# Kernel optimization log

Measured on AMD Instinct MI355X. Metric: run time of the kernel, lower is better.

The kernel has to match this reference:

```python
import jax, jax.numpy as jnp
import numpy as np

SIGMA = 1.0          # influence distance of kernel points
KERNEL_RADIUS = 1.0  # radius within which kernel points live


def setup_inputs() -> dict:
    key = jax.random.key(0)
    k0, k1, k2, k3, k4 = jax.random.split(key, 5)
    B, M, K_NB, D_IN, D_OUT, K_PTS = 4, 16384, 32, 64, 64, 15
    X = jax.random.normal(k0, (B, M, 3), dtype=jnp.float32)          # point coords
    F = jax.random.normal(k1, (B, M, D_IN), dtype=jnp.float32)        # point features
    N = jax.random.randint(k2, (B, M, K_NB), 0, M)                    # neighbor indices
    Q = jax.random.uniform(k3, (K_PTS, 3), minval=-KERNEL_RADIUS,
                           maxval=KERNEL_RADIUS, dtype=jnp.float32)   # kernel points
    W = jax.random.normal(k4, (K_PTS, D_IN, D_OUT), dtype=jnp.float32) * 0.05
    return {"X": X, "F": F, "N": N, "Q": Q, "W": W}


def reference(X, F, N, Q, W):
    # Gather neighbor coordinates and features: [B, M, k, 3] / [B, M, k, d_in]
    gather = jax.vmap(lambda a, idx: a[idx])
    Xn = gather(X, N)
    Fn = gather(F, N)
    # Relative neighbor positions w.r.t. each center point
    r = Xn - X[:, :, None, :]                                  # [B, M, k, 3]
    # Distance of each relative position to each kernel point
    d = jnp.linalg.norm(r[:, :, :, None, :] - Q, axis=-1)      # [B, M, k, Kp]
    # Linear correlation influence (KPConv)
    h = jnp.maximum(0.0, 1.0 - d / SIGMA)                      # [B, M, k, Kp]
    # Distance-weighted neighbor aggregation per kernel point
    Fk = jnp.einsum('bmkp,bmkd->bmpd', h, Fn)                  # [B, M, Kp, d_in]
    # Per-kernel-point linear maps, summed over kernel points
    return jnp.einsum('bmpd,pde->bme', Fk, W)                  # [B, M, d_out]
```

## Files before the change

### kernel.cpp

```cpp
#include <hip/hip_runtime.h>
#include <hip/hip_bf16.h>


#define BATCH 4
#define MPTS  16384
#define KNB   32
#define DIN   64
#define DOUT  64
#define KP    15
#define K2P   1024
#define KSTEPS (K2P/32)
#define ROWB  (K2P*2)
#define PTS   (BATCH*MPTS)
#define PPB   16
#define NBLK  (PTS/PPB)
#define WBELEMS (K2P*DOUT)

typedef __bf16 bf16x8 __attribute__((ext_vector_type(8)));
typedef float  f32x4  __attribute__((ext_vector_type(4)));
typedef unsigned short u16x8 __attribute__((ext_vector_type(8)));

static __device__ __forceinline__ unsigned short f2b(float x) {
    __bf16 h = (__bf16)x;
    return __builtin_bit_cast(unsigned short, h);
}

__global__ void prep_wb(const float* __restrict__ W, unsigned short* __restrict__ wb) {
    int idx = blockIdx.x * 256 + threadIdx.x;
    if (idx >= WBELEMS) return;
    int i    = idx & 7;
    int lane = (idx >> 3) & 63;
    int ks   = (idx >> 9) & 31;
    int et   = idx >> 14;
    int kap  = ks * 32 + ((lane >> 4) << 3) + i;
    int n = kap >> 6;
    int g = (kap >> 4) & 3;
    int t = (kap >> 2) & 3;
    int r = kap & 3;
    int p = g * 4 + r;
    int d = n * 4 + t;
    int e = et * 16 + (lane & 15);
    float v = (p < KP) ? W[(p * DIN + d) * DOUT + e] : 0.f;
    wb[idx] = f2b(v);
}

__global__ void f2bf_kernel(const float* __restrict__ src, unsigned short* __restrict__ dst, int n8) {
    int i = blockIdx.x * 256 + threadIdx.x;
    if (i >= n8) return;
    const float4* s = reinterpret_cast<const float4*>(src) + (size_t)i * 2;
    float4 a = s[0], b = s[1];
    u16x8 o;
    o[0] = f2b(a.x); o[1] = f2b(a.y); o[2] = f2b(a.z); o[3] = f2b(a.w);
    o[4] = f2b(b.x); o[5] = f2b(b.y); o[6] = f2b(b.z); o[7] = f2b(b.w);
    *(reinterpret_cast<u16x8*>(dst) + i) = o;
}

__global__ __launch_bounds__(256, 4)
void kpconv_main(const float* __restrict__ X, const unsigned short* __restrict__ FB,
                 const int* __restrict__ NB, const float* __restrict__ Q,
                 const unsigned short* __restrict__ WB, float* __restrict__ OUT) {
    __shared__ unsigned short fk[16 * K2P];
    __shared__ float4 stg[4][4][KNB];

    const int tid  = threadIdx.x;
    const int wv   = tid >> 6;
    const int lane = tid & 63;
    const int g16  = lane >> 4;
    const int r16  = lane & 15;

    float qx = 1.0e3f, qy = 0.f, qz = 0.f;
    if (r16 < KP) { qx = Q[r16 * 3 + 0]; qy = Q[r16 * 3 + 1]; qz = Q[r16 * 3 + 2]; }
    const float qq   = qx * qx + qy * qy + qz * qz;
    const float nq2x = -2.f * qx, nq2y = -2.f * qy, nq2z = -2.f * qz;

    const int bid     = blockIdx.x;
    const int base_pt = (bid & 7) * (PTS / 8) + (bid >> 3) * PPB;
    const int boff    = (base_pt >> 14) * MPTS;
    const int pid0    = base_pt + wv * 4;

    #pragma unroll
    for (int e = 0; e < 2; ++e) {
        int ent = lane + e * 64;
        int j = ent >> 5, k = ent & 31;
        int pid = pid0 + j;
        int nb  = NB[(size_t)pid * KNB + k];
        int gidx = boff + nb;
        const float* xn = X + (size_t)gidx * 3;
        const float* xc = X + (size_t)pid * 3;
        float rx = xn[0] - xc[0];
        float ry = xn[1] - xc[1];
        float rz = xn[2] - xc[2];
        float rr = fmaf(rx, rx, fmaf(ry, ry, rz * rz));
        int slot = (k & 24) | ((k ^ (k >> 3)) & 7);
        stg[wv][j][slot] = make_float4(rx, ry, rz, rr);
    }

    union U { uint2 d; unsigned short s[4]; };
    U L[2][8];

    auto issue_gather = [&](int j, U* Lj) {
        const int* nbp = NB + (size_t)(pid0 + j) * KNB + g16 * 8;
        int4 a = *reinterpret_cast<const int4*>(nbp);
        int4 b = *reinterpret_cast<const int4*>(nbp + 4);
        int g[8] = {a.x, a.y, a.z, a.w, b.x, b.y, b.z, b.w};
        #pragma unroll
        for (int i = 0; i < 8; ++i)
            Lj[i].d = *reinterpret_cast<const uint2*>(
                FB + ((size_t)(boff + g[i]) << 6) + (r16 << 2));
    };

    issue_gather(0, L[0]);
    issue_gather(1, L[1]);

    #pragma unroll
    for (int j = 0; j < 4; ++j) {
        const int row = wv * 4 + j;

        bf16x8 ah;
        #pragma unroll
        for (int i = 0; i < 8; ++i) {
            float4 rv = stg[wv][j][g16 * 8 + (i ^ g16)];
            float d2 = fmaf(rv.x, nq2x, fmaf(rv.y, nq2y, fmaf(rv.z, nq2z, rv.w + qq)));
            d2 = fmaxf(d2, 0.f);
            ah[i] = (__bf16)fmaxf(1.f - __builtin_amdgcn_sqrtf(d2), 0.f);
        }

        bf16x8 bfr[4];
        #pragma unroll
        for (int t = 0; t < 4; ++t)
            #pragma unroll
            for (int i = 0; i < 8; ++i)
                bfr[t][i] = __builtin_bit_cast(__bf16, L[j & 1][i].s[t]);

        if (j < 2) issue_gather(j + 2, L[j & 1]);

        const f32x4 z = {0.f, 0.f, 0.f, 0.f};
        f32x4 accs[4];
        #pragma unroll
        for (int t = 0; t < 4; ++t)
            accs[t] = __builtin_amdgcn_mfma_f32_16x16x32_bf16(ah, bfr[t], z, 0, 0, 0);

        bf16x8 w0, w1;
        #pragma unroll
        for (int r = 0; r < 4; ++r) {
            w0[r]     = (__bf16)accs[0][r];
            w0[4 + r] = (__bf16)accs[1][r];
            w1[r]     = (__bf16)accs[2][r];
            w1[4 + r] = (__bf16)accs[3][r];
        }
        int swz  = (row & 7) ^ (r16 & 7);
        int off0 = row * ROWB + (r16 * 8 + ((g16 * 2 + 0) ^ swz)) * 16;
        int off1 = row * ROWB + (r16 * 8 + ((g16 * 2 + 1) ^ swz)) * 16;
        *reinterpret_cast<bf16x8*>(reinterpret_cast<char*>(fk) + off0) = w0;
        *reinterpret_cast<bf16x8*>(reinterpret_cast<char*>(fk) + off1) = w1;
    }

    __syncthreads();

    const unsigned short* wbp = WB + ((size_t)(wv * KSTEPS) * 64 + lane) * 8;
    asm volatile("" : "+v"(wbp));

    f32x4 o = {0.f, 0.f, 0.f, 0.f};
    #pragma unroll
    for (int ks = 0; ks < KSTEPS; ++ks) {
        bf16x8 b = *reinterpret_cast<const bf16x8*>(wbp + ks * 512);
        int stored = (ks * 4 + g16) ^ (r16 & 7) ^ ((ks >> 1) & 7);
        bf16x8 a = *reinterpret_cast<const bf16x8*>(
            reinterpret_cast<const char*>(fk) + r16 * ROWB + stored * 16);
        o = __builtin_amdgcn_mfma_f32_16x16x32_bf16(a, b, o, 0, 0, 0);
    }

    #pragma unroll
    for (int r = 0; r < 4; ++r) {
        int pid = base_pt + g16 * 4 + r;
        OUT[(size_t)pid * DOUT + wv * 16 + r16] = o[r];
    }
}

extern "C" void kernel_launch(void* const* d_in, const int* in_sizes, int n_in,
                              void* d_out, int out_size, void* d_ws, size_t ws_size,
                              hipStream_t stream) {
    const float* X = (const float*)d_in[0];
    const float* F = (const float*)d_in[1];
    const int*   N = (const int*)d_in[2];
    const float* Q = (const float*)d_in[3];
    const float* W = (const float*)d_in[4];
    float* OUT = (float*)d_out;
    unsigned short* WB = (unsigned short*)d_ws;
    unsigned short* FB = WB + WBELEMS;

    prep_wb<<<(WBELEMS + 255) / 256, 256, 0, stream>>>(W, WB);

    const int n8 = PTS * DIN / 8;
    f2bf_kernel<<<(n8 + 255) / 256, 256, 0, stream>>>(F, FB, n8);

    kpconv_main<<<NBLK, 256, 0, stream>>>(X, FB, N, Q, WB, OUT);
}
```

Measured before the change: 63.45 us.

## Process two point tiles per block with cross-tile prefetch, merge prep kernels

Each block of the main kernel now handles two 16-point tiles. While the second-stage MFMA loop over the W matrix runs for the first tile, it prefetches the neighbor indices, coordinates and feature gathers for the second tile, aiming to hide gather latency behind compute. The two preprocessing kernels (W reordering and F bf16 conversion) are merged into one launch to save a kernel launch. This costs more registers and one extra barrier per block, and halves the grid size, which may reduce occupancy.

```diff
diff --git a/kernel.cpp b/kernel.cpp
--- a/kernel.cpp
+++ b/kernel.cpp
@@ -12,9 +12,11 @@
 #define KSTEPS (K2P/32)
 #define ROWB  (K2P*2)
 #define PTS   (BATCH*MPTS)
-#define PPB   16
+#define PPB   32
 #define NBLK  (PTS/PPB)
 #define WBELEMS (K2P*DOUT)
+#define WBBLK (WBELEMS/256)
+#define FBBLK (PTS*DIN/8/256)
 
 typedef __bf16 bf16x8 __attribute__((ext_vector_type(8)));
 typedef float  f32x4  __attribute__((ext_vector_type(4)));
@@ -25,34 +27,34 @@
     return __builtin_bit_cast(unsigned short, h);
 }
 
-__global__ void prep_wb(const float* __restrict__ W, unsigned short* __restrict__ wb) {
-    int idx = blockIdx.x * 256 + threadIdx.x;
-    if (idx >= WBELEMS) return;
-    int i    = idx & 7;
-    int lane = (idx >> 3) & 63;
-    int ks   = (idx >> 9) & 31;
-    int et   = idx >> 14;
-    int kap  = ks * 32 + ((lane >> 4) << 3) + i;
-    int n = kap >> 6;
-    int g = (kap >> 4) & 3;
-    int t = (kap >> 2) & 3;
-    int r = kap & 3;
-    int p = g * 4 + r;
-    int d = n * 4 + t;
-    int e = et * 16 + (lane & 15);
-    float v = (p < KP) ? W[(p * DIN + d) * DOUT + e] : 0.f;
-    wb[idx] = f2b(v);
-}
-
-__global__ void f2bf_kernel(const float* __restrict__ src, unsigned short* __restrict__ dst, int n8) {
-    int i = blockIdx.x * 256 + threadIdx.x;
-    if (i >= n8) return;
-    const float4* s = reinterpret_cast<const float4*>(src) + (size_t)i * 2;
-    float4 a = s[0], b = s[1];
-    u16x8 o;
-    o[0] = f2b(a.x); o[1] = f2b(a.y); o[2] = f2b(a.z); o[3] = f2b(a.w);
-    o[4] = f2b(b.x); o[5] = f2b(b.y); o[6] = f2b(b.z); o[7] = f2b(b.w);
-    *(reinterpret_cast<u16x8*>(dst) + i) = o;
+__global__ void prep_all(const float* __restrict__ W, const float* __restrict__ F,
+                         unsigned short* __restrict__ wb, unsigned short* __restrict__ fb) {
+    int bid = blockIdx.x;
+    if (bid < WBBLK) {
+        int idx = bid * 256 + threadIdx.x;
+        int i    = idx & 7;
+        int lane = (idx >> 3) & 63;
+        int ks   = (idx >> 9) & 31;
+        int et   = idx >> 14;
+        int kap  = ks * 32 + ((lane >> 4) << 3) + i;
+        int n = kap >> 6;
+        int g = (kap >> 4) & 3;
+        int t = (kap >> 2) & 3;
+        int r = kap & 3;
+        int p = g * 4 + r;
+        int d = n * 4 + t;
+        int e = et * 16 + (lane & 15);
+        float v = (p < KP) ? W[(p * DIN + d) * DOUT + e] : 0.f;
+        wb[idx] = f2b(v);
+    } else {
+        int i = (bid - WBBLK) * 256 + threadIdx.x;
+        const float4* s = reinterpret_cast<const float4*>(F) + (size_t)i * 2;
+        float4 a = s[0], b = s[1];
+        u16x8 o;
+        o[0] = f2b(a.x); o[1] = f2b(a.y); o[2] = f2b(a.z); o[3] = f2b(a.w);
+        o[4] = f2b(b.x); o[5] = f2b(b.y); o[6] = f2b(b.z); o[7] = f2b(b.w);
+        *(reinterpret_cast<u16x8*>(fb) + i) = o;
+    }
 }
 
 __global__ __launch_bounds__(256, 4)
@@ -62,6 +64,8 @@
     __shared__ unsigned short fk[16 * K2P];
     __shared__ float4 stg[4][4][KNB];
 
+    char* const fkb = reinterpret_cast<char*>(fk);
+
     const int tid  = threadIdx.x;
     const int wv   = tid >> 6;
     const int lane = tid & 63;
@@ -76,30 +80,12 @@
     const int bid     = blockIdx.x;
     const int base_pt = (bid & 7) * (PTS / 8) + (bid >> 3) * PPB;
     const int boff    = (base_pt >> 14) * MPTS;
-    const int pid0    = base_pt + wv * 4;
-
-    #pragma unroll
-    for (int e = 0; e < 2; ++e) {
-        int ent = lane + e * 64;
-        int j = ent >> 5, k = ent & 31;
-        int pid = pid0 + j;
-        int nb  = NB[(size_t)pid * KNB + k];
-        int gidx = boff + nb;
-        const float* xn = X + (size_t)gidx * 3;
-        const float* xc = X + (size_t)pid * 3;
-        float rx = xn[0] - xc[0];
-        float ry = xn[1] - xc[1];
-        float rz = xn[2] - xc[2];
-        float rr = fmaf(rx, rx, fmaf(ry, ry, rz * rz));
-        int slot = (k & 24) | ((k ^ (k >> 3)) & 7);
-        stg[wv][j][slot] = make_float4(rx, ry, rz, rr);
-    }
 
     union U { uint2 d; unsigned short s[4]; };
     U L[2][8];
 
-    auto issue_gather = [&](int j, U* Lj) {
-        const int* nbp = NB + (size_t)(pid0 + j) * KNB + g16 * 8;
+    auto issue_gather = [&](int pid_j, U* Lj) {
+        const int* nbp = NB + (size_t)pid_j * KNB + g16 * 8;
         int4 a = *reinterpret_cast<const int4*>(nbp);
         int4 b = *reinterpret_cast<const int4*>(nbp + 4);
         int g[8] = {a.x, a.y, a.z, a.w, b.x, b.y, b.z, b.w};
@@ -109,71 +95,147 @@
                 FB + ((size_t)(boff + g[i]) << 6) + (r16 << 2));
     };
 
-    issue_gather(0, L[0]);
-    issue_gather(1, L[1]);
+    auto stage_stg = [&](int tp) {
+        #pragma unroll
+        for (int e = 0; e < 2; ++e) {
+            int ent = lane + e * 64;
+            int j = ent >> 5, k = ent & 31;
+            int pid = tp + wv * 4 + j;
+            int nb  = NB[(size_t)pid * KNB + k];
+            int gidx = boff + nb;
+            const float* xn = X + (size_t)gidx * 3;
+            const float* xc = X + (size_t)pid * 3;
+            float rx = xn[0] - xc[0];
+            float ry = xn[1] - xc[1];
+            float rz = xn[2] - xc[2];
+            float rr = fmaf(rx, rx, fmaf(ry, ry, rz * rz));
+            int slot = (k & 24) | ((k ^ (k >> 3)) & 7);
+            stg[wv][j][slot] = make_float4(rx, ry, rz, rr);
+        }
+    };
+
+    stage_stg(base_pt);
+    issue_gather(base_pt + wv * 4 + 0, L[0]);
+    issue_gather(base_pt + wv * 4 + 1, L[1]);
 
     #pragma unroll
-    for (int j = 0; j < 4; ++j) {
-        const int row = wv * 4 + j;
-
-        bf16x8 ah;
-        #pragma unroll
-        for (int i = 0; i < 8; ++i) {
-            float4 rv = stg[wv][j][g16 * 8 + (i ^ g16)];
-            float d2 = fmaf(rv.x, nq2x, fmaf(rv.y, nq2y, fmaf(rv.z, nq2z, rv.w + qq)));
-            d2 = fmaxf(d2, 0.f);
-            ah[i] = (__bf16)fmaxf(1.f - __builtin_amdgcn_sqrtf(d2), 0.f);
-        }
-
-        bf16x8 bfr[4];
-        #pragma unroll
-        for (int t = 0; t < 4; ++t)
-            #pragma unroll
-            for (int i = 0; i < 8; ++i)
-                bfr[t][i] = __builtin_bit_cast(__bf16, L[j & 1][i].s[t]);
-
-        if (j < 2) issue_gather(j + 2, L[j & 1]);
-
-        const f32x4 z = {0.f, 0.f, 0.f, 0.f};
-        f32x4 accs[4];
-        #pragma unroll
-        for (int t = 0; t < 4; ++t)
-            accs[t] = __builtin_amdgcn_mfma_f32_16x16x32_bf16(ah, bfr[t], z, 0, 0, 0);
-
-        bf16x8 w0, w1;
+    for (int tile = 0; tile < 2; ++tile) {
+        const int tp   = base_pt + tile * 16;
+        const int pid0 = tp + wv * 4;
+
+        #pragma unroll
+        for (int j = 0; j < 4; ++j) {
+            const int row = wv * 4 + j;
+
+            bf16x8 ah;
+            #pragma unroll
+            for (int i = 0; i < 8; ++i) {
+                float4 rv = stg[wv][j][g16 * 8 + (i ^ g16)];
+                float d2 = fmaf(rv.x, nq2x, fmaf(rv.y, nq2y, fmaf(rv.z, nq2z, rv.w + qq)));
+                d2 = fmaxf(d2, 0.f);
+                ah[i] = (__bf16)fmaxf(1.f - __builtin_amdgcn_sqrtf(d2), 0.f);
+            }
+
+            bf16x8 bfr[4];
+            #pragma unroll
+            for (int t = 0; t < 4; ++t)
+                #pragma unroll
+                for (int i = 0; i < 8; ++i)
+                    bfr[t][i] = __builtin_bit_cast(__bf16, L[j & 1][i].s[t]);
+
+            if (j < 2) issue_gather(pid0 + j + 2, L[j & 1]);
+
+            const f32x4 z = {0.f, 0.f, 0.f, 0.f};
+            f32x4 accs[4];
+            #pragma unroll
+            for (int t = 0; t < 4; ++t)
+                accs[t] = __builtin_amdgcn_mfma_f32_16x16x32_bf16(ah, bfr[t], z, 0, 0, 0);
+
+            bf16x8 w0, w1;
+            #pragma unroll
+            for (int r = 0; r < 4; ++r) {
+                w0[r]     = (__bf16)accs[0][r];
+                w0[4 + r] = (__bf16)accs[1][r];
+                w1[r]     = (__bf16)accs[2][r];
+                w1[4 + r] = (__bf16)accs[3][r];
+            }
+            int swz  = (row & 7) ^ (r16 & 7);
+            int off0 = row * ROWB + (r16 * 8 + ((g16 * 2 + 0) ^ swz)) * 16;
+            int off1 = row * ROWB + (r16 * 8 + ((g16 * 2 + 1) ^ swz)) * 16;
+            *reinterpret_cast<bf16x8*>(fkb + off0) = w0;
+            *reinterpret_cast<bf16x8*>(fkb + off1) = w1;
+        }
+
+        __syncthreads();
+
+        int   A_nb[2];
+        float A_xn[2][3], A_xc[2][3];
+        int4  A_ga[2][2];
+        if (tile == 0) {
+            const int tp1 = base_pt + 16;
+            #pragma unroll
+            for (int e = 0; e < 2; ++e) {
+                int ent = lane + e * 64;
+                int j = ent >> 5, k = ent & 31;
+                int pid = tp1 + wv * 4 + j;
+                int nb  = NB[(size_t)pid * KNB + k];
+                A_nb[e] = nb;
+                const float* xn = X + (size_t)(boff + nb) * 3;
+                const float* xc = X + (size_t)pid * 3;
+                #pragma unroll
+                for (int c = 0; c < 3; ++c) { A_xn[e][c] = xn[c]; A_xc[e][c] = xc[c]; }
+            }
+            #pragma unroll
+            for (int j2 = 0; j2 < 2; ++j2) {
+                const int* nbp = NB + (size_t)(tp1 + wv * 4 + j2) * KNB + g16 * 8;
+                A_ga[j2][0] = *reinterpret_cast<const int4*>(nbp);
+                A_ga[j2][1] = *reinterpret_cast<const int4*>(nbp + 4);
+            }
+            __builtin_amdgcn_sched_barrier(0);
+        }
+
+        const unsigned short* wbp = WB + ((size_t)(wv * KSTEPS) * 64 + lane) * 8;
+        asm volatile("" : "+v"(wbp));
+
+        f32x4 o = {0.f, 0.f, 0.f, 0.f};
+        #pragma unroll
+        for (int ks = 0; ks < KSTEPS; ++ks) {
+            bf16x8 b = *reinterpret_cast<const bf16x8*>(wbp + ks * 512);
+            int stored = (ks * 4 + g16) ^ (r16 & 7) ^ ((ks >> 1) & 7);
+            bf16x8 a = *reinterpret_cast<const bf16x8*>(fkb + r16 * ROWB + stored * 16);
+            o = __builtin_amdgcn_mfma_f32_16x16x32_bf16(a, b, o, 0, 0, 0);
+        }
+
+        if (tile == 0) {
+            #pragma unroll
+            for (int e = 0; e < 2; ++e) {
+                int ent = lane + e * 64;
+                int j = ent >> 5, k = ent & 31;
+                float rx = A_xn[e][0] - A_xc[e][0];
+                float ry = A_xn[e][1] - A_xc[e][1];
+                float rz = A_xn[e][2] - A_xc[e][2];
+                float rr = fmaf(rx, rx, fmaf(ry, ry, rz * rz));
+                int slot = (k & 24) | ((k ^ (k >> 3)) & 7);
+                stg[wv][j][slot] = make_float4(rx, ry, rz, rr);
+            }
+            #pragma unroll
+            for (int j2 = 0; j2 < 2; ++j2) {
+                int g[8] = {A_ga[j2][0].x, A_ga[j2][0].y, A_ga[j2][0].z, A_ga[j2][0].w,
+                            A_ga[j2][1].x, A_ga[j2][1].y, A_ga[j2][1].z, A_ga[j2][1].w};
+                #pragma unroll
+                for (int i = 0; i < 8; ++i)
+                    L[j2][i].d = *reinterpret_cast<const uint2*>(
+                        FB + ((size_t)(boff + g[i]) << 6) + (r16 << 2));
+            }
+        }
+
         #pragma unroll
         for (int r = 0; r < 4; ++r) {
-            w0[r]     = (__bf16)accs[0][r];
-            w0[4 + r] = (__bf16)accs[1][r];
-            w1[r]     = (__bf16)accs[2][r];
-            w1[4 + r] = (__bf16)accs[3][r];
-        }
-        int swz  = (row & 7) ^ (r16 & 7);
-        int off0 = row * ROWB + (r16 * 8 + ((g16 * 2 + 0) ^ swz)) * 16;
-        int off1 = row * ROWB + (r16 * 8 + ((g16 * 2 + 1) ^ swz)) * 16;
-        *reinterpret_cast<bf16x8*>(reinterpret_cast<char*>(fk) + off0) = w0;
-        *reinterpret_cast<bf16x8*>(reinterpret_cast<char*>(fk) + off1) = w1;
-    }
-
-    __syncthreads();
-
-    const unsigned short* wbp = WB + ((size_t)(wv * KSTEPS) * 64 + lane) * 8;
-    asm volatile("" : "+v"(wbp));
-
-    f32x4 o = {0.f, 0.f, 0.f, 0.f};
-    #pragma unroll
-    for (int ks = 0; ks < KSTEPS; ++ks) {
-        bf16x8 b = *reinterpret_cast<const bf16x8*>(wbp + ks * 512);
-        int stored = (ks * 4 + g16) ^ (r16 & 7) ^ ((ks >> 1) & 7);
-        bf16x8 a = *reinterpret_cast<const bf16x8*>(
-            reinterpret_cast<const char*>(fk) + r16 * ROWB + stored * 16);
-        o = __builtin_amdgcn_mfma_f32_16x16x32_bf16(a, b, o, 0, 0, 0);
-    }
-
-    #pragma unroll
-    for (int r = 0; r < 4; ++r) {
-        int pid = base_pt + g16 * 4 + r;
-        OUT[(size_t)pid * DOUT + wv * 16 + r16] = o[r];
+            int pid = tp + g16 * 4 + r;
+            OUT[(size_t)pid * DOUT + wv * 16 + r16] = o[r];
+        }
+
+        if (tile == 0) __syncthreads();
     }
 }
 
@@ -189,10 +251,6 @@
     unsigned short* WB = (unsigned short*)d_ws;
     unsigned short* FB = WB + WBELEMS;
 
-    prep_wb<<<(WBELEMS + 255) / 256, 256, 0, stream>>>(W, WB);
-
-    const int n8 = PTS * DIN / 8;
-    f2bf_kernel<<<(n8 + 255) / 256, 256, 0, stream>>>(F, FB, n8);
-
+    prep_all<<<WBBLK + FBBLK, 256, 0, stream>>>(W, F, WB, FB);
     kpconv_main<<<NBLK, 256, 0, stream>>>(X, FB, N, Q, WB, OUT);
 }
```

Measured after the change: 61.27 us. -3.4%, faster.
